# Kernel tuning notes

Hardware: AMD Instinct MI355X
Metric: run time of the kernel (lower is better)

Reference implementation:

```python
import jax, jax.numpy as jnp
import numpy as np

B, T, C = 2, 2048, 1024
H, D = 16, 64  # n_head, head_size = C // H


def setup_inputs() -> dict:
    key = jax.random.key(0)
    ks = jax.random.split(key, 6)
    s = 1.0 / np.sqrt(C)
    x = jax.random.normal(ks[0], (B, T, C), dtype=jnp.float32)
    Wq = jax.random.normal(ks[1], (C, C), dtype=jnp.float32) * s
    Wk = jax.random.normal(ks[2], (C, C), dtype=jnp.float32) * s
    Wv = jax.random.normal(ks[3], (C, C), dtype=jnp.float32) * s
    Wp = jax.random.normal(ks[4], (C, C), dtype=jnp.float32) * s
    bp = jnp.zeros((C,), dtype=jnp.float32)
    return {"x": x, "Wq": Wq, "Wk": Wk, "Wv": Wv, "Wp": Wp, "bp": bp}


def _feature_map(x):
    # F.elu(x) + 1.0
    return jnp.where(x > 0, x + 1.0, jnp.exp(x))


def reference(x, Wq, Wk, Wv, Wp, bp):
    Bx, Tx, Cx = x.shape
    # q,k,v projections (nn.Linear with weight W applies x @ W.T)
    q = (x @ Wq.T).reshape(Bx, Tx, H, D).transpose(0, 2, 1, 3)  # bhtd
    k = (x @ Wk.T).reshape(Bx, Tx, H, D).transpose(0, 2, 1, 3)
    v = (x @ Wv.T).reshape(Bx, Tx, H, D).transpose(0, 2, 1, 3)
    qp = _feature_map(q)
    kp = _feature_map(k)
    # cumulative outer-product context: (B,H,T,D,D)
    kv_cum = jnp.cumsum(jnp.einsum('bhsd,bhsv->bhsdv', kp, v), axis=2)
    ksum_cum = jnp.cumsum(kp, axis=2)  # (B,H,T,D)
    num = jnp.einsum('bhsd,bhsdv->bhsv', qp, kv_cum)
    den = jnp.einsum('bhsd,bhsd->bhs', qp, ksum_cum)[..., None] + 1e-6
    y = (num / den).transpose(0, 2, 1, 3).reshape(Bx, Tx, Cx)
    out = y @ Wp.T + bp  # dropout(p=0) is identity
    new_kv = kv_cum[:, :, -1]
    new_ksum = ksum_cum[:, :, -1]
    return (out, new_kv, new_ksum)
```

## Files before the change

### kernel.cpp

```cpp
#include <hip/hip_runtime.h>
#include <math.h>

#define BB 2
#define TT 2048
#define CC 1024
#define HH 16
#define DD 64
#define MM (BB*TT)
#define LCH 128
#define NCH (TT/LCH)
#define BHH (BB*HH)

#define OUT_OFF_KV   4194304
#define OUT_OFF_KSUM 4325376
#define MB 1048576

typedef unsigned int u32;
typedef unsigned short u16;
typedef __attribute__((ext_vector_type(8))) short s16x8;
typedef __attribute__((ext_vector_type(8))) unsigned short us8;
typedef __attribute__((ext_vector_type(4))) float f32x4;

__device__ __forceinline__ float fmap(float x) {
    return x > 0.0f ? x + 1.0f : expf(x);
}
__device__ __forceinline__ u16 bf16r(float f) {
    u32 u = __float_as_uint(f);
    u += 0x7fffu + ((u >> 16) & 1u);
    return (u16)(u >> 16);
}
__device__ __forceinline__ float bf2f(u16 u) {
    return __uint_as_float(((u32)u) << 16);
}
__device__ __forceinline__ void gload16(const void* g, void* l) {
    __builtin_amdgcn_global_load_lds(
        (const __attribute__((address_space(1))) u32*)g,
        (__attribute__((address_space(3))) u32*)l, 16, 0, 0);
}

__global__ __launch_bounds__(256)
void f2bf_all(const float* __restrict__ x,
              const float* __restrict__ Wq, const float* __restrict__ Wk,
              const float* __restrict__ Wv, const float* __restrict__ Wp,
              u16* __restrict__ xbf, u16* __restrict__ wbf)
{
    const int i = blockIdx.x * 256 + threadIdx.x;
    const float* src;
    u16* dst;
    int off;
    if (i < 524288) {
        src = x; dst = xbf; off = i;
    } else {
        const int j = i - 524288;
        const int sel = j >> 17;
        off = j & 131071;
        src = (sel == 0) ? Wq : (sel == 1) ? Wk : (sel == 2) ? Wv : Wp;
        dst = wbf + ((size_t)sel << 20);
    }
    const float4 a = ((const float4*)src)[off*2];
    const float4 b = ((const float4*)src)[off*2 + 1];
    us8 p;
    p[0]=bf16r(a.x); p[1]=bf16r(a.y); p[2]=bf16r(a.z); p[3]=bf16r(a.w);
    p[4]=bf16r(b.x); p[5]=bf16r(b.y); p[6]=bf16r(b.z); p[7]=bf16r(b.w);
    ((us8*)dst)[off] = p;
}

__device__ __forceinline__ void read_a(const char* LB, int abase, int wm, int lr, int lg4,
                                       s16x8 (&af)[4][2])
{
    #pragma unroll
    for (int mi = 0; mi < 4; ++mi) {
        const int r = wm*64 + mi*16 + lr;
        #pragma unroll
        for (int ks = 0; ks < 2; ++ks) {
            const int gg = (ks*4 + lg4) ^ (r & 7);
            af[mi][ks] = *(const s16x8*)(LB + abase + r*128 + gg*16);
        }
    }
}
__device__ __forceinline__ void read_b(const char* LB, int bbase, int wn, int lr, int lg4,
                                       s16x8 (&bv)[2][2])
{
    #pragma unroll
    for (int ni = 0; ni < 2; ++ni) {
        const int r = wn*32 + ni*16 + lr;
        #pragma unroll
        for (int ks = 0; ks < 2; ++ks) {
            const int gg = (ks*4 + lg4) ^ (r & 7);
            bv[ni][ks] = *(const s16x8*)(LB + bbase + r*128 + gg*16);
        }
    }
}
__device__ __forceinline__ void phase_mfma(const s16x8 (&af)[4][2], const s16x8 (&bv)[2][2],
                                           f32x4 (&acc)[4][2])
{
    #pragma unroll
    for (int mi = 0; mi < 4; ++mi)
        #pragma unroll
        for (int ni = 0; ni < 2; ++ni)
            #pragma unroll
            for (int ks = 0; ks < 2; ++ks)
                acc[mi][ni] = __builtin_amdgcn_mfma_f32_16x16x32_bf16(
                    af[mi][ks], bv[ni][ks], acc[mi][ni], 0, 0, 0);
}

__global__ __launch_bounds__(512, 2)
void lca_gemm_qkv8(const u16* __restrict__ A, const u16* __restrict__ Wall,
                   u16* __restrict__ qp, u16* __restrict__ kp,
                   u16* __restrict__ kt, u16* __restrict__ vt)
{
    extern __shared__ char LB[];
    const int tid  = threadIdx.x;
    const int lane = tid & 63;
    const int wid  = tid >> 6;
    const int wm   = wid >> 2;
    const int wn   = wid & 3;
    const int bm0  = blockIdx.y * 256;
    const int bn0g = blockIdx.x * 256;
    const int sel  = bn0g >> 10;
    const int nn0  = bn0g & (CC-1);
    const u16* W = Wall + ((size_t)sel << 20);
    const int NT = CC / 64;

    const int srow = (wid << 3) + (lane >> 3);
    const int sg   = lane & 7;
    auto STAGE = [&](const u16* G, int ldsbase) {
        #pragma unroll
        for (int j = 0; j < 2; ++j) {
            const int r  = j*64 + srow;
            const int gs = sg ^ (r & 7);
            gload16(G + (size_t)r * CC + gs*8,
                    LB + ldsbase + (size_t)(j*64 + (wid<<3))*128);
        }
    };
    #define LDSA(slot,h) (((slot)*2 + (h))*16384)
    #define LDSB(slot,h) (65536 + ((slot)*2 + (h))*16384)

    f32x4 acc[4][4][2];
    #pragma unroll
    for (int q = 0; q < 4; ++q)
        #pragma unroll
        for (int mi = 0; mi < 4; ++mi)
            #pragma unroll
            for (int ni = 0; ni < 2; ++ni)
                acc[q][mi][ni] = (f32x4){0.f, 0.f, 0.f, 0.f};

    STAGE(A + (size_t)(bm0      ) * CC + 0,  LDSA(0,0));
    STAGE(A + (size_t)(bm0 + 128) * CC + 0,  LDSA(0,1));
    STAGE(W + (size_t)(nn0      ) * CC + 0,  LDSB(0,0));
    STAGE(W + (size_t)(nn0 + 128) * CC + 0,  LDSB(0,1));
    STAGE(A + (size_t)(bm0      ) * CC + 64, LDSA(1,0));
    STAGE(W + (size_t)(nn0      ) * CC + 64, LDSB(1,0));
    asm volatile("s_waitcnt vmcnt(4)" ::: "memory");
    __builtin_amdgcn_s_barrier();

    const int lr  = lane & 15;
    const int lg4 = lane >> 4;

    s16x8 afr[4][2];
    s16x8 b0r[2][2];
    s16x8 b1r[2][2];

    for (int t = 0; t < NT; ++t) {
        const int slot = t & 1;

        { const int tt = t + 1;
          if (tt < NT) STAGE(A + (size_t)(bm0 + 128)*CC + tt*64, LDSA(tt&1,1)); }
        read_a(LB, LDSA(slot,0), wm, lr, lg4, afr);
        read_b(LB, LDSB(slot,0), wn, lr, lg4, b0r);
        __builtin_amdgcn_sched_barrier(0);
        if (t < NT-1) asm volatile("s_waitcnt vmcnt(6)" ::: "memory");
        else          asm volatile("s_waitcnt vmcnt(4)" ::: "memory");
        __builtin_amdgcn_s_barrier();
        asm volatile("s_waitcnt lgkmcnt(0)" ::: "memory");
        __builtin_amdgcn_sched_barrier(0);
        __builtin_amdgcn_s_setprio(1);
        phase_mfma(afr, b0r, acc[0]);
        __builtin_amdgcn_s_setprio(0);
        __builtin_amdgcn_sched_barrier(0);
        __builtin_amdgcn_s_barrier();

        { const int tt = t + 1;
          if (tt < NT) STAGE(W + (size_t)(nn0 + 128)*CC + tt*64, LDSB(tt&1,1)); }
        read_b(LB, LDSB(slot,1), wn, lr, lg4, b1r);
        __builtin_amdgcn_sched_barrier(0);
        if (t < NT-1) asm volatile("s_waitcnt vmcnt(6)" ::: "memory");
        else          asm volatile("s_waitcnt vmcnt(0)" ::: "memory");
        __builtin_amdgcn_s_barrier();
        asm volatile("s_waitcnt lgkmcnt(0)" ::: "memory");
        __builtin_amdgcn_sched_barrier(0);
        __builtin_amdgcn_s_setprio(1);
        phase_mfma(afr, b1r, acc[1]);
        __builtin_amdgcn_s_setprio(0);
        __builtin_amdgcn_sched_barrier(0);
        __builtin_amdgcn_s_barrier();

        { const int tt = t + 2;
          if (tt < NT) STAGE(A + (size_t)(bm0      )*CC + tt*64, LDSA(tt&1,0)); }
        read_a(LB, LDSA(slot,1), wm, lr, lg4, afr);
        __builtin_amdgcn_sched_barrier(0);
        if (t < NT-1) asm volatile("s_waitcnt vmcnt(6)" ::: "memory");
        __builtin_amdgcn_s_barrier();
        asm volatile("s_waitcnt lgkmcnt(0)" ::: "memory");
        __builtin_amdgcn_sched_barrier(0);
        __builtin_amdgcn_s_setprio(1);
        phase_mfma(afr, b0r, acc[2]);
        __builtin_amdgcn_s_setprio(0);
        __builtin_amdgcn_sched_barrier(0);
        __builtin_amdgcn_s_barrier();

        { const int tt = t + 2;
          if (tt < NT) STAGE(W + (size_t)(nn0      )*CC + tt*64, LDSB(tt&1,0)); }
        __builtin_amdgcn_sched_barrier(0);
        if (t < NT-1) asm volatile("s_waitcnt vmcnt(6)" ::: "memory");
        __builtin_amdgcn_s_barrier();
        __builtin_amdgcn_sched_barrier(0);
        __builtin_amdgcn_s_setprio(1);
        phase_mfma(afr, b1r, acc[3]);
        __builtin_amdgcn_s_setprio(0);
        __builtin_amdgcn_sched_barrier(0);
        __builtin_amdgcn_s_barrier();
    }

    #pragma unroll
    for (int q = 0; q < 4; ++q) {
        const int mh = q >> 1, nh = q & 1;
        #pragma unroll
        for (int mi = 0; mi < 4; ++mi) {
            #pragma unroll
            for (int ni = 0; ni < 2; ++ni) {
                const int coln = nn0 + nh*128 + wn*32 + ni*16 + lr;
                const int rb   = bm0 + mh*128 + wm*64 + mi*16 + lg4*4;
                const int h = coln >> 6, d = coln & (DD-1);
                const int b = rb >> 11, t0 = rb & (TT-1);
                u16 bvv[4];
                #pragma unroll
                for (int r = 0; r < 4; ++r) {
                    float val = acc[q][mi][ni][r];
                    if (sel != 2) val = fmap(val);
                    bvv[r] = bf16r(val);
                }
                if (sel == 0) {
                    u16* p = qp + (((size_t)(b*HH + h)) * TT + t0) * DD + d;
                    #pragma unroll
                    for (int r = 0; r < 4; ++r) p[(size_t)r * DD] = bvv[r];
                } else {
                    const int ch = t0 >> 7, tc = t0 & (LCH-1);
                    u16* pt = (sel == 1 ? kt : vt)
                            + (((size_t)((b*HH + h)*NCH + ch)) * DD + d) * LCH + tc;
                    *(ushort4*)pt = make_ushort4(bvv[0], bvv[1], bvv[2], bvv[3]);
                    if (sel == 1) {
                        u16* p = kp + (((size_t)(b*HH + h)) * TT + t0) * DD + d;
                        #pragma unroll
                        for (int r = 0; r < 4; ++r) p[(size_t)r * DD] = bvv[r];
                    }
                }
            }
        }
    }
    #undef LDSA
    #undef LDSB
}

__global__ __launch_bounds__(256)
void lca_gemm_out(const u16* __restrict__ A, const u16* __restrict__ W,
                  const float* __restrict__ bias, float* __restrict__ out)
{
    __shared__ short As[2][4096];
    __shared__ short Bs2[2][2048];
    const int tid  = threadIdx.x;
    const int lane = tid & 63;
    const int wid  = tid >> 6;
    const int bm0 = blockIdx.y * 128;
    const int bn0 = blockIdx.x * 64;
    const int wm = wid >> 1, wn = wid & 1;

    const int rsA = wid*32 + (lane >> 2);
    const int rsB = wid*16 + (lane >> 2);
    const int kc  = (lane & 3) * 8;

    f32x4 acc[4][2];
    #pragma unroll
    for (int i = 0; i < 4; ++i)
        #pragma unroll
        for (int j = 0; j < 2; ++j)
            acc[i][j] = (f32x4){0.f, 0.f, 0.f, 0.f};

    const int rA = wm*64 + (lane & 15);
    const int rB = wn*32 + (lane & 15);
    const int kk = (lane >> 4) * 8;

    #pragma unroll
    for (int j = 0; j < 2; ++j)
        gload16(A + (size_t)(bm0 + rsA + j*16) * CC + kc, &As[0][wid*1024 + j*512]);
    gload16(W + (size_t)(bn0 + rsB) * CC + kc, &Bs2[0][wid*512]);
    __syncthreads();

    int cur = 0;
    for (int k0 = 0; k0 < CC; k0 += 32) {
        if (k0 + 32 < CC) {
            #pragma unroll
            for (int j = 0; j < 2; ++j)
                gload16(A + (size_t)(bm0 + rsA + j*16) * CC + k0 + 32 + kc, &As[cur^1][wid*1024 + j*512]);
            gload16(W + (size_t)(bn0 + rsB) * CC + k0 + 32 + kc, &Bs2[cur^1][wid*512]);
        }

        s16x8 af[4], bf[2];
        #pragma unroll
        for (int mi = 0; mi < 4; ++mi) af[mi] = *(const s16x8*)(&As[cur][(rA + mi*16)*32 + kk]);
        #pragma unroll
        for (int ni = 0; ni < 2; ++ni) bf[ni] = *(const s16x8*)(&Bs2[cur][(rB + ni*16)*32 + kk]);
        #pragma unroll
        for (int mi = 0; mi < 4; ++mi)
            #pragma unroll
            for (int ni = 0; ni < 2; ++ni)
                acc[mi][ni] = __builtin_amdgcn_mfma_f32_16x16x32_bf16(af[mi], bf[ni], acc[mi][ni], 0, 0, 0);

        __syncthreads();
        cur ^= 1;
    }

    #pragma unroll
    for (int mi = 0; mi < 4; ++mi) {
        #pragma unroll
        for (int ni = 0; ni < 2; ++ni) {
            const int col = bn0 + wn*32 + ni*16 + (lane & 15);
            const int rb  = bm0 + wm*64 + mi*16 + (lane >> 4)*4;
            const float bb = bias[col];
            #pragma unroll
            for (int r = 0; r < 4; ++r)
                out[(size_t)(rb + r) * CC + col] = acc[mi][ni][r] + bb;
        }
    }
}

__global__ __launch_bounds__(256)
void lca_pass1(const u16* __restrict__ kt, const u16* __restrict__ vt,
               float* __restrict__ Sloc, float* __restrict__ ksloc)
{
    const int wid = threadIdx.x >> 6, lane = threadIdx.x & 63;
    const int c = blockIdx.x * 4 + wid, bh = blockIdx.y;
    const u16* kg = kt + ((size_t)bh * NCH + c) * DD * LCH;
    const u16* vg = vt + ((size_t)bh * NCH + c) * DD * LCH;
    const int lr = lane & 15;
    const int lk = (lane >> 4) * 8;

    f32x4 acc[4][4];
    #pragma unroll
    for (int i = 0; i < 4; ++i)
        #pragma unroll
        for (int j = 0; j < 4; ++j)
            acc[i][j] = (f32x4){0.f, 0.f, 0.f, 0.f};

    #pragma unroll
    for (int ks = 0; ks < 4; ++ks) {
        const int k = ks*32 + lk;
        s16x8 af[4], bf[4];
        #pragma unroll
        for (int mi = 0; mi < 4; ++mi) af[mi] = *(const s16x8*)(kg + (size_t)(mi*16 + lr)*LCH + k);
        #pragma unroll
        for (int ni = 0; ni < 4; ++ni) bf[ni] = *(const s16x8*)(vg + (size_t)(ni*16 + lr)*LCH + k);
        #pragma unroll
        for (int mi = 0; mi < 4; ++mi)
            #pragma unroll
            for (int ni = 0; ni < 4; ++ni)
                acc[mi][ni] = __builtin_amdgcn_mfma_f32_16x16x32_bf16(af[mi], bf[ni], acc[mi][ni], 0, 0, 0);
    }

    float* So = Sloc + ((size_t)bh * NCH + c) * (DD*DD);
    #pragma unroll
    for (int mi = 0; mi < 4; ++mi)
        #pragma unroll
        for (int ni = 0; ni < 4; ++ni) {
            const int e = ni*16 + lr;
            #pragma unroll
            for (int r = 0; r < 4; ++r) {
                const int d = mi*16 + (lane >> 4)*4 + r;
                So[(size_t)d * DD + e] = acc[mi][ni][r];
            }
        }

    float s = 0.0f;
    #pragma unroll
    for (int i = 0; i < 16; ++i) {
        s16x8 dv = *(const s16x8*)(kg + (size_t)lane * LCH + i*8);
        #pragma unroll
        for (int j = 0; j < 8; ++j) s += bf2f((u16)dv[j]);
    }
    ksloc[((size_t)bh * NCH + c) * DD + lane] = s;
}

__global__ __launch_bounds__(256)
void lca_pass2(const float* __restrict__ Sloc, const float* __restrict__ ksloc,
               u16* __restrict__ pst, float* __restrict__ pksx,
               float* __restrict__ out)
{
    const int bh = blockIdx.x;
    const int tid = threadIdx.x;
    const int d0 = (tid >> 4) * 4;
    const int e0 = (tid & 15) * 4;

    float run[4][4] = {};
    for (int c = 0; c < NCH; ++c) {
        u16* P = pst + ((size_t)bh * NCH + c) * (DD*DD);
        #pragma unroll
        for (int i = 0; i < 4; ++i)
            #pragma unroll
            for (int j = 0; j < 4; ++j)
                P[(size_t)(e0 + j) * DD + (d0 + i)] = bf16r(run[i][j]);
        const float* S = Sloc + ((size_t)bh * NCH + c) * (DD*DD);
        #pragma unroll
        for (int i = 0; i < 4; ++i) {
            const float4 t4 = *(const float4*)(S + (size_t)(d0 + i) * DD + e0);
            run[i][0] += t4.x; run[i][1] += t4.y; run[i][2] += t4.z; run[i][3] += t4.w;
        }
    }
    float* nkv = out + OUT_OFF_KV + (size_t)bh * (DD*DD);
    #pragma unroll
    for (int i = 0; i < 4; ++i)
        *(float4*)(nkv + (size_t)(d0 + i) * DD + e0) =
            make_float4(run[i][0], run[i][1], run[i][2], run[i][3]);

    if (tid < DD) {
        float r = 0.0f;
        for (int c = 0; c < NCH; ++c) {
            pksx[((size_t)bh * NCH + c) * DD + tid] = r;
            r += ksloc[((size_t)bh * NCH + c) * DD + tid];
        }
        out[OUT_OFF_KSUM + (size_t)bh * DD + tid] = r;
    }
}

__global__ __launch_bounds__(256)
void lca_pass3(const u16* __restrict__ qp, const u16* __restrict__ kp,
               const u16* __restrict__ vt, const u16* __restrict__ pst,
               const float* __restrict__ pksx, u16* __restrict__ ybf)
{
    __shared__ short SA[16384];
    __shared__ short VS[8192];
    __shared__ short PS[4096];
    __shared__ float pks_s[DD];
    __shared__ float den_s[LCH];

    char* SAb = (char*)SA;
    char* VSb = (char*)VS;
    char* PSb = (char*)PS;

    const int c = blockIdx.x, bh = blockIdx.y;
    const int tid = threadIdx.x;
    const int lane = tid & 63, wid = tid >> 6;

    const u16* qg = qp + ((size_t)bh * TT + (size_t)c * LCH) * DD;
    const u16* kg = kp + ((size_t)bh * TT + (size_t)c * LCH) * DD;
    const u16* vg = vt + ((size_t)bh * NCH + c) * DD * LCH;
    const u16* pg = pst + ((size_t)bh * NCH + c) * (DD*DD);

    for (int i = tid; i < 1024; i += 256) {
        const int row = i >> 3, cc = i & 7;
        const s16x8 dv = *(const s16x8*)(qg + (size_t)row*DD + cc*8);
        *(s16x8*)(SAb + ((row*128 + cc*16) ^ ((row & 7) << 4))) = dv;
    }
    for (int i = tid; i < 1024; i += 256) {
        const int row = i >> 3, cc = i & 7;
        const s16x8 dv = *(const s16x8*)(kg + (size_t)row*DD + cc*8);
        *(s16x8*)(SAb + 16384 + ((row*128 + cc*16) ^ ((row & 7) << 4))) = dv;
    }
    for (int i = tid; i < 1024; i += 256) {
        const int row = i >> 4, cc = i & 15;
        const s16x8 dv = *(const s16x8*)(vg + (size_t)row*LCH + cc*8);
        *(s16x8*)(VSb + ((row*256 + cc*16) ^ ((row & 7) << 4))) = dv;
    }
    for (int i = tid; i < 512; i += 256) {
        const int row = i >> 3, cc = i & 7;
        const s16x8 dv = *(const s16x8*)(pg + (size_t)row*DD + cc*8);
        *(s16x8*)(PSb + ((row*128 + cc*16) ^ ((row & 7) << 4))) = dv;
    }
    if (tid < DD) pks_s[tid] = pksx[((size_t)bh * NCH + c) * DD + tid];
    __syncthreads();

    if (tid < LCH) {
        const int t = tid;
        float s = 1e-6f;
        #pragma unroll
        for (int cc = 0; cc < 8; ++cc) {
            const s16x8 dv = *(const s16x8*)(SAb + ((t*128 + cc*16) ^ ((t & 7) << 4)));
            #pragma unroll
            for (int j = 0; j < 8; ++j) s += bf2f((u16)dv[j]) * pks_s[cc*8 + j];
        }
        den_s[t] = s;
    }

    const int wrow0 = wid * 32;
    const int lr = lane & 15;
    const int lg = lane >> 4;
    const int lk = lg * 8;

    f32x4 sacc[2][8];
    #pragma unroll
    for (int mi = 0; mi < 2; ++mi)
        #pragma unroll
        for (int ni = 0; ni < 8; ++ni)
            sacc[mi][ni] = (f32x4){0.f, 0.f, 0.f, 0.f};

    #pragma unroll
    for (int ks = 0; ks < 2; ++ks) {
        const int k2 = (ks*32 + lk) * 2;
        s16x8 af[2];
        #pragma unroll
        for (int mi = 0; mi < 2; ++mi) {
            const int row = wrow0 + mi*16 + lr;
            af[mi] = *(const s16x8*)(SAb + ((row*128 + k2) ^ ((row & 7) << 4)));
        }
        #pragma unroll
        for (int ni = 0; ni < 8; ++ni) {
            const int rowb = ni*16 + lr;
            const s16x8 bf = *(const s16x8*)(SAb + 16384 + ((rowb*128 + k2) ^ ((rowb & 7) << 4)));
            sacc[0][ni] = __builtin_amdgcn_mfma_f32_16x16x32_bf16(af[0], bf, sacc[0][ni], 0, 0, 0);
            sacc[1][ni] = __builtin_amdgcn_mfma_f32_16x16x32_bf16(af[1], bf, sacc[1][ni], 0, 0, 0);
        }
    }

    f32x4 pv[2][4];
    #pragma unroll
    for (int mi = 0; mi < 2; ++mi)
        #pragma unroll
        for (int ni = 0; ni < 4; ++ni)
            pv[mi][ni] = (f32x4){0.f, 0.f, 0.f, 0.f};

    #pragma unroll
    for (int ks = 0; ks < 2; ++ks) {
        const int k2 = (ks*32 + lk) * 2;
        s16x8 af[2];
        #pragma unroll
        for (int mi = 0; mi < 2; ++mi) {
            const int row = wrow0 + mi*16 + lr;
            af[mi] = *(const s16x8*)(SAb + ((row*128 + k2) ^ ((row & 7) << 4)));
        }
        #pragma unroll
        for (int ni = 0; ni < 4; ++ni) {
            const int rowb = ni*16 + lr;
            const s16x8 bf = *(const s16x8*)(PSb + ((rowb*128 + k2) ^ ((rowb & 7) << 4)));
            pv[0][ni] = __builtin_amdgcn_mfma_f32_16x16x32_bf16(af[0], bf, pv[0][ni], 0, 0, 0);
            pv[1][ni] = __builtin_amdgcn_mfma_f32_16x16x32_bf16(af[1], bf, pv[1][ni], 0, 0, 0);
        }
    }
    __syncthreads();

    #pragma unroll
    for (int mi = 0; mi < 2; ++mi) {
        float dr[4] = {0.f, 0.f, 0.f, 0.f};
        #pragma unroll
        for (int ni = 0; ni < 8; ++ni) {
            const int tp = ni*16 + lr;
            #pragma unroll
            for (int r = 0; r < 4; ++r) {
                const int t = wrow0 + mi*16 + lg*4 + r;
                const float v = (tp <= t) ? sacc[mi][ni][r] : 0.f;
                dr[r] += v;
                *(u16*)(SAb + ((t*256 + tp*2) ^ ((t & 7) << 4))) = bf16r(v);
            }
        }
        #pragma unroll
        for (int r = 0; r < 4; ++r) {
            float s = dr[r];
            s += __shfl_xor(s, 1); s += __shfl_xor(s, 2);
            s += __shfl_xor(s, 4); s += __shfl_xor(s, 8);
            if (lr == 0) {
                const int t = wrow0 + mi*16 + lg*4 + r;
                den_s[t] += s;
            }
        }
    }
    __syncthreads();

    #pragma unroll
    for (int ks = 0; ks < 4; ++ks) {
        const int k2 = (ks*32 + lk) * 2;
        s16x8 af[2];
        #pragma unroll
        for (int mi = 0; mi < 2; ++mi) {
            const int row = wrow0 + mi*16 + lr;
            af[mi] = *(const s16x8*)(SAb + ((row*256 + k2) ^ ((row & 7) << 4)));
        }
        #pragma unroll
        for (int ni = 0; ni < 4; ++ni) {
            const int rowb = ni*16 + lr;
            const s16x8 bf = *(const s16x8*)(VSb + ((rowb*256 + k2) ^ ((rowb & 7) << 4)));
            pv[0][ni] = __builtin_amdgcn_mfma_f32_16x16x32_bf16(af[0], bf, pv[0][ni], 0, 0, 0);
            pv[1][ni] = __builtin_amdgcn_mfma_f32_16x16x32_bf16(af[1], bf, pv[1][ni], 0, 0, 0);
        }
    }

    const int b = bh >> 4, h = bh & (HH-1);
    #pragma unroll
    for (int mi = 0; mi < 2; ++mi)
        #pragma unroll
        for (int ni = 0; ni < 4; ++ni) {
            const int e = ni*16 + lr;
            #pragma unroll
            for (int r = 0; r < 4; ++r) {
                const int t = wrow0 + mi*16 + lg*4 + r;
                const float y = pv[mi][ni][r] / den_s[t];
                ybf[((size_t)(b*TT) + (size_t)c*LCH + t) * CC + h*DD + e] = bf16r(y);
            }
        }
}

extern "C" void kernel_launch(void* const* d_in, const int* in_sizes, int n_in,
                              void* d_out, int out_size, void* d_ws, size_t ws_size,
                              hipStream_t stream) {
    const float* x  = (const float*)d_in[0];
    const float* Wq = (const float*)d_in[1];
    const float* Wk = (const float*)d_in[2];
    const float* Wv = (const float*)d_in[3];
    const float* Wp = (const float*)d_in[4];
    const float* bp = (const float*)d_in[5];
    float* out = (float*)d_out;
    char* ws = (char*)d_ws;

    u16*   xbf  = (u16*)(ws + 0);
    u16*   Wbf  = (u16*)(ws + (size_t)8*MB);
    u16*   qp   = (u16*)(ws + (size_t)16*MB);
    u16*   kp   = (u16*)(ws + (size_t)24*MB);
    u16*   kt   = (u16*)(ws + (size_t)32*MB);
    u16*   vt   = (u16*)(ws + (size_t)40*MB);
    u16*   ybf  = (u16*)(ws + (size_t)48*MB);
    float* Sl   = (float*)(ws + (size_t)56*MB);
    float* ksl  = (float*)(ws + (size_t)64*MB);
    float* pksx = (float*)(ws + (size_t)64*MB + 131072);
    u16*   pst  = (u16*)(ws + (size_t)65*MB);

    (void)hipFuncSetAttribute((const void*)lca_gemm_qkv8,
                              hipFuncAttributeMaxDynamicSharedMemorySize, 131072);

    f2bf_all<<<4096, 256, 0, stream>>>(x, Wq, Wk, Wv, Wp, xbf, Wbf);

    lca_gemm_qkv8<<<dim3(3*CC/256, MM/256), 512, 131072, stream>>>(xbf, Wbf, qp, kp, kt, vt);

    lca_pass1<<<dim3(NCH/4, BHH), 256, 0, stream>>>(kt, vt, Sl, ksl);
    lca_pass2<<<BHH, 256, 0, stream>>>(Sl, ksl, pst, pksx, out);
    lca_pass3<<<dim3(NCH, BHH), 256, 0, stream>>>(qp, kp, vt, pst, pksx, ybf);

    lca_gemm_out<<<dim3(CC/64, MM/128), 256, 0, stream>>>(ybf, Wbf + ((size_t)3 << 20), bp, out);
}
```

Baseline: 127.1 us.

## Prefetch LDS fragments one phase ahead to overlap reads with MFMA

Restructures the 4-phase GEMM main loop so LDS fragment reads for the next phase (and the next k-tile's first A/B fragments) are issued before the current phase's MFMAs. It uses double register fragments (afr0/afr1) and partial lgkmcnt waits, and drops one barrier per phase. The aim is to hide LDS read latency behind matrix math. In exchange it raises register pressure, and the waitcnt and barrier accounting becomes more delicate around slot reuse.

```diff
diff --git a/kernel.cpp b/kernel.cpp
--- a/kernel.cpp
+++ b/kernel.cpp
@@ -157,66 +157,60 @@
     const int lr  = lane & 15;
     const int lg4 = lane >> 4;
 
-    s16x8 afr[4][2];
-    s16x8 b0r[2][2];
-    s16x8 b1r[2][2];
+    s16x8 afr0[4][2], afr1[4][2], b0r[2][2], b1r[2][2];
+    read_a(LB, LDSA(0,0), wm, lr, lg4, afr0);
+    read_b(LB, LDSB(0,0), wn, lr, lg4, b0r);
 
     for (int t = 0; t < NT; ++t) {
-        const int slot = t & 1;
-
-        { const int tt = t + 1;
-          if (tt < NT) STAGE(A + (size_t)(bm0 + 128)*CC + tt*64, LDSA(tt&1,1)); }
-        read_a(LB, LDSA(slot,0), wm, lr, lg4, afr);
-        read_b(LB, LDSB(slot,0), wn, lr, lg4, b0r);
+        const int slot  = t & 1;
+        const int nslot = slot ^ 1;
+
+        if (t+1 < NT) STAGE(A + (size_t)(bm0 + 128)*CC + (t+1)*64, LDSA(nslot,1));
+        read_b(LB, LDSB(slot,1), wn, lr, lg4, b1r);
         __builtin_amdgcn_sched_barrier(0);
         if (t < NT-1) asm volatile("s_waitcnt vmcnt(6)" ::: "memory");
-        else          asm volatile("s_waitcnt vmcnt(4)" ::: "memory");
+        asm volatile("s_waitcnt lgkmcnt(4)" ::: "memory");
+        __builtin_amdgcn_sched_barrier(0);
+        __builtin_amdgcn_s_setprio(1);
+        phase_mfma(afr0, b0r, acc[0]);
+        __builtin_amdgcn_s_setprio(0);
+        __builtin_amdgcn_sched_barrier(0);
         __builtin_amdgcn_s_barrier();
+
+        if (t+1 < NT) STAGE(W + (size_t)(nn0 + 128)*CC + (t+1)*64, LDSB(nslot,1));
+        read_a(LB, LDSA(slot,1), wm, lr, lg4, afr1);
+        __builtin_amdgcn_sched_barrier(0);
+        if (t < NT-1) asm volatile("s_waitcnt vmcnt(6)" ::: "memory");
+        asm volatile("s_waitcnt lgkmcnt(8)" ::: "memory");
+        __builtin_amdgcn_sched_barrier(0);
+        __builtin_amdgcn_s_setprio(1);
+        phase_mfma(afr0, b1r, acc[1]);
+        __builtin_amdgcn_s_setprio(0);
+        __builtin_amdgcn_sched_barrier(0);
+        __builtin_amdgcn_s_barrier();
+
+        if (t+2 < NT) STAGE(A + (size_t)(bm0)*CC + (t+2)*64, LDSA(slot,0));
+        __builtin_amdgcn_sched_barrier(0);
+        if (t < NT-1) asm volatile("s_waitcnt vmcnt(4)" ::: "memory");
         asm volatile("s_waitcnt lgkmcnt(0)" ::: "memory");
         __builtin_amdgcn_sched_barrier(0);
         __builtin_amdgcn_s_setprio(1);
-        phase_mfma(afr, b0r, acc[0]);
+        phase_mfma(afr1, b0r, acc[2]);
         __builtin_amdgcn_s_setprio(0);
         __builtin_amdgcn_sched_barrier(0);
         __builtin_amdgcn_s_barrier();
 
-        { const int tt = t + 1;
-          if (tt < NT) STAGE(W + (size_t)(nn0 + 128)*CC + tt*64, LDSB(tt&1,1)); }
-        read_b(LB, LDSB(slot,1), wn, lr, lg4, b1r);
-        __builtin_amdgcn_sched_barrier(0);
-        if (t < NT-1) asm volatile("s_waitcnt vmcnt(6)" ::: "memory");
-        else          asm volatile("s_waitcnt vmcnt(0)" ::: "memory");
-        __builtin_amdgcn_s_barrier();
-        asm volatile("s_waitcnt lgkmcnt(0)" ::: "memory");
+        if (t+2 < NT) STAGE(W + (size_t)(nn0)*CC + (t+2)*64, LDSB(slot,0));
+        if (t+1 < NT) {
+            read_a(LB, LDSA(nslot,0), wm, lr, lg4, afr0);
+            read_b(LB, LDSB(nslot,0), wn, lr, lg4, b0r);
+        }
+        __builtin_amdgcn_sched_barrier(0);
+        if (t < NT-2)       asm volatile("s_waitcnt vmcnt(4)" ::: "memory");
+        else if (t == NT-2) asm volatile("s_waitcnt vmcnt(0)" ::: "memory");
         __builtin_amdgcn_sched_barrier(0);
         __builtin_amdgcn_s_setprio(1);
-        phase_mfma(afr, b1r, acc[1]);
-        __builtin_amdgcn_s_setprio(0);
-        __builtin_amdgcn_sched_barrier(0);
-        __builtin_amdgcn_s_barrier();
-
-        { const int tt = t + 2;
-          if (tt < NT) STAGE(A + (size_t)(bm0      )*CC + tt*64, LDSA(tt&1,0)); }
-        read_a(LB, LDSA(slot,1), wm, lr, lg4, afr);
-        __builtin_amdgcn_sched_barrier(0);
-        if (t < NT-1) asm volatile("s_waitcnt vmcnt(6)" ::: "memory");
-        __builtin_amdgcn_s_barrier();
-        asm volatile("s_waitcnt lgkmcnt(0)" ::: "memory");
-        __builtin_amdgcn_sched_barrier(0);
-        __builtin_amdgcn_s_setprio(1);
-        phase_mfma(afr, b0r, acc[2]);
-        __builtin_amdgcn_s_setprio(0);
-        __builtin_amdgcn_sched_barrier(0);
-        __builtin_amdgcn_s_barrier();
-
-        { const int tt = t + 2;
-          if (tt < NT) STAGE(W + (size_t)(nn0      )*CC + tt*64, LDSB(tt&1,0)); }
-        __builtin_amdgcn_sched_barrier(0);
-        if (t < NT-1) asm volatile("s_waitcnt vmcnt(6)" ::: "memory");
-        __builtin_amdgcn_s_barrier();
-        __builtin_amdgcn_sched_barrier(0);
-        __builtin_amdgcn_s_setprio(1);
-        phase_mfma(afr, b1r, acc[3]);
+        phase_mfma(afr1, b1r, acc[3]);
         __builtin_amdgcn_s_setprio(0);
         __builtin_amdgcn_sched_barrier(0);
         __builtin_amdgcn_s_barrier();
```

Measured after the change: 124.8 us. No clear change (-1.8%).
